# Optimization experiments

Measured on AMD Instinct MI355X. Metric: run time of the kernel, lower is better.

## Reference

```python
import jax, jax.numpy as jnp
import numpy as np
from jax import lax

B, N, C, RED = 8, 2048, 1024, 4
GN_EPS = 1e-5


def setup_inputs() -> dict:
    key = jax.random.key(0)
    ks = jax.random.split(key, 8)
    s = lambda k, shp, sc: jax.random.normal(k, shp, jnp.float32) * sc
    return dict(
        x=jax.random.normal(ks[0], (B, N, C), jnp.float32),
        qkv_w=s(ks[1], (C, 3 * C), 0.02),
        c1=jnp.float32(0.01 ** 2),
        c2=jnp.float32(0.03 ** 2),
        conv1_w=s(ks[2], (4, 1, 3), 0.3),      # OIH
        gn_g=jnp.ones(4, jnp.float32),
        gn_b=jnp.zeros(4, jnp.float32),
        conv2_w=s(ks[3], (1, 4, 3), 0.3),      # OIH
        conv2_b=jnp.zeros(1, jnp.float32),
        ch_w1=s(ks[4], (C, C // RED), 0.02),
        ch_b1=jnp.zeros(C // RED, jnp.float32),
        ch_w2=s(ks[5], (C // RED, C), 0.02),
        ch_b2=jnp.zeros(C, jnp.float32),
        proj_w=s(ks[6], (C, C), 0.02),
        proj_b=jnp.zeros(C, jnp.float32),
    )


def _conv1d(x, w):  # x:[B,Cin,N], w:[O,I,3], pad=1
    return lax.conv_general_dilated(x, w, (1,), [(1, 1)],
                                    dimension_numbers=('NCH', 'OIH', 'NCH'))


def _ode_func(A, conv1_w, gn_g, gn_b, conv2_w, conv2_b):
    # A: [B,N] -> Conv1d(1,4) -> GroupNorm(2,4) -> ReLU -> Conv1d(4,1)
    h = _conv1d(A[:, None, :], conv1_w)                 # [B,4,N]
    b, _, n = h.shape
    hg = h.reshape(b, 2, 2, n)                          # 2 groups of 2 channels
    mu = hg.mean((2, 3), keepdims=True)
    var = hg.var((2, 3), keepdims=True)
    h = ((hg - mu) * lax.rsqrt(var + GN_EPS)).reshape(b, 4, n)
    h = jax.nn.relu(h * gn_g[None, :, None] + gn_b[None, :, None])
    y = _conv1d(h, conv2_w) + conv2_b[None, :, None]    # [B,1,N]
    return y[:, 0, :]


def reference(x, qkv_w, c1, c2, conv1_w, gn_g, gn_b, conv2_w, conv2_b,
              ch_w1, ch_b1, ch_w2, ch_b2, proj_w, proj_b):
    Bx, Nx, Cx = x.shape
    qkv = (x @ qkv_w).reshape(Bx, Nx, 3, Cx)
    q, k, v = qkv[..., 0, :], qkv[..., 1, :], qkv[..., 2, :]

    # SSIM-style per-token statistics over the channel dim
    mu_q = q.mean(-1, keepdims=True)
    mu_k = k.mean(-1, keepdims=True)
    dq, dk = q - mu_q, k - mu_k
    inv_cm1 = 1.0 / (Cx - 1)
    sigma_qk = (dq * dk).sum(-1, keepdims=True) * inv_cm1
    sigma_q2 = (dq * dq).sum(-1, keepdims=True) * inv_cm1
    sigma_k2 = (dk * dk).sum(-1, keepdims=True) * inv_cm1
    num = (2 * mu_q * mu_k + c1) * (2 * sigma_qk + c2)
    den = (mu_q ** 2 + mu_k ** 2 + c1) * (sigma_q2 + sigma_k2 + c2)
    attn_base = ((num / (den + 1e-7)) ** 2)[..., 0]     # [B,N]

    # explicit-Euler integration over t = linspace(0,1,2) -> one step, dt=1
    steps = 2
    ts = jnp.linspace(0.0, 1.0, steps)
    dts = ts[1:] - ts[:-1]

    def step(A, dt):
        return A + dt * _ode_func(A, conv1_w, gn_g, gn_b, conv2_w, conv2_b), None

    A, _ = lax.scan(step, attn_base, dts)
    final_a = jax.nn.sigmoid(A)                         # [B,N]
    weights = jax.nn.softmax(final_a, axis=1)           # softmax over tokens

    # channel gating from mean token
    m = x.mean(axis=1, keepdims=True)                   # [B,1,C]
    ch_w = jax.nn.sigmoid(jax.nn.relu(m @ ch_w1 + ch_b1) @ ch_w2 + ch_b2)

    out_low = weights[..., None] * v * ch_w             # [B,N,C]
    return out_low @ proj_w + proj_b
```

## Files before the change

kernel.cpp:

```cpp
#include <hip/hip_runtime.h>

typedef __attribute__((ext_vector_type(8))) short short8;
typedef __attribute__((ext_vector_type(4))) short short4v;
typedef __attribute__((ext_vector_type(4))) float floatx4;

__device__ __forceinline__ unsigned short f2bf(float f) {
    unsigned u = __float_as_uint(f);
    u = u + 0x7fffu + ((u >> 16) & 1u);
    return (unsigned short)(u >> 16);
}

__device__ __forceinline__ void gl_lds16(const void* g, void* l) {
    __builtin_amdgcn_global_load_lds((const __attribute__((address_space(1))) void*)g,
                                     (__attribute__((address_space(3))) void*)l, 16, 0, 0);
}

__global__ __launch_bounds__(256) void convmean_kernel(const float* __restrict__ x,
                                                       short* __restrict__ xb,
                                                       float* __restrict__ part) {
    int bid = blockIdx.x;
    int b = bid >> 6, nch = bid & 63;
    int tid = threadIdx.x;
    size_t base = ((size_t)b * 2048 + nch * 32) * 1024;
    float s0 = 0.f, s1 = 0.f, s2 = 0.f, s3 = 0.f;
    int c0 = tid * 4;
    for (int r = 0; r < 32; r++) {
        const float* rp = x + base + (size_t)r * 1024 + c0;
        float4 v = *(const float4*)rp;
        s0 += v.x; s1 += v.y; s2 += v.z; s3 += v.w;
        short4v o;
        o[0] = (short)f2bf(v.x); o[1] = (short)f2bf(v.y);
        o[2] = (short)f2bf(v.z); o[3] = (short)f2bf(v.w);
        *(short4v*)(xb + base + (size_t)r * 1024 + c0) = o;
    }
    float* pp = part + ((size_t)b * 64 + nch) * 1024 + c0;
    float4 ps; ps.x = s0; ps.y = s1; ps.z = s2; ps.w = s3;
    *(float4*)pp = ps;
}

__global__ __launch_bounds__(256) void transpose_conv_kernel(const float* __restrict__ w_qkv,
                                                             short* __restrict__ qkvT,
                                                             const float* __restrict__ w_proj,
                                                             short* __restrict__ projT) {
    __shared__ float t[64][65];
    int bx = blockIdx.x;
    const float* in; short* out; int C; bool is_qkv;
    int c0, r0 = blockIdx.y * 64;
    if (bx < 48) { in = w_qkv; out = qkvT; C = 3072; c0 = bx * 64; is_qkv = true; }
    else         { in = w_proj; out = projT; C = 1024; c0 = (bx - 48) * 64; is_qkv = false; }
    int tid = threadIdx.x;
#pragma unroll
    for (int l = 0; l < 16; l++) {
        int idx = l * 256 + tid;
        int rr = idx >> 6, cc = idx & 63;
        t[rr][cc] = in[(size_t)(r0 + rr) * C + c0 + cc];
    }
    __syncthreads();
#pragma unroll
    for (int l = 0; l < 16; l++) {
        int idx = l * 256 + tid;
        int rr = idx >> 6, cc = idx & 63;
        int ro = c0 + rr;
        int rnew = ro;
        if (is_qkv) {
            if (ro < 1024) rnew = 2 * ro;
            else if (ro < 2048) rnew = 2 * (ro - 1024) + 1;
        }
        out[(size_t)rnew * 1024 + r0 + cc] = (short)f2bf(t[cc][rr]);
    }
}

__global__ __launch_bounds__(256) void ch_kernel(const float* __restrict__ part,
                                                 const float* __restrict__ w1,
                                                 const float* __restrict__ b1,
                                                 const float* __restrict__ w2,
                                                 const float* __restrict__ b2,
                                                 float* __restrict__ ch) {
    int b = blockIdx.x >> 3, cg = blockIdx.x & 7;
    int tid = threadIdx.x;
    __shared__ float mrow[1024];
    __shared__ float hid[256];
    for (int i = tid; i < 1024; i += 256) {
        float s = 0.f;
        for (int j = 0; j < 64; j++) s += part[((size_t)b * 64 + j) * 1024 + i];
        mrow[i] = s * (1.f / 2048.f);
    }
    __syncthreads();
    {
        float s0 = 0.f, s1 = 0.f, s2 = 0.f, s3 = 0.f;
        for (int i = 0; i < 1024; i += 4) {
            s0 += mrow[i] * w1[(size_t)i * 256 + tid];
            s1 += mrow[i + 1] * w1[(size_t)(i + 1) * 256 + tid];
            s2 += mrow[i + 2] * w1[(size_t)(i + 2) * 256 + tid];
            s3 += mrow[i + 3] * w1[(size_t)(i + 3) * 256 + tid];
        }
        hid[tid] = fmaxf((s0 + s1) + (s2 + s3) + b1[tid], 0.f);
    }
    __syncthreads();
    if (tid < 128) {
        int c = cg * 128 + tid;
        float s0 = 0.f, s1 = 0.f, s2 = 0.f, s3 = 0.f;
        for (int j = 0; j < 256; j += 4) {
            s0 += hid[j] * w2[(size_t)j * 1024 + c];
            s1 += hid[j + 1] * w2[(size_t)(j + 1) * 1024 + c];
            s2 += hid[j + 2] * w2[(size_t)(j + 2) * 1024 + c];
            s3 += hid[j + 3] * w2[(size_t)(j + 3) * 1024 + c];
        }
        float s = (s0 + s1) + (s2 + s3) + b2[c];
        ch[(size_t)b * 1024 + c] = 1.f / (1.f + expf(-s));
    }
}


#define LDB4()                                                                          \
    {                                                                                   \
        _Pragma("unroll")                                                               \
        for (int jj = 0; jj < 4; jj++)                                                  \
            bfr[jj] = *(const short8*)(Bs_ + (wn * 64 + jj * 16 + ar) * 32 + swq);      \
    }

#define PH(qq, STAGE)                                                                   \
    {                                                                                   \
        short8 a0 = *(const short8*)(As_ + (wm * 128 + ((qq)*2 + 0) * 16 + ar) * 32 + swq); \
        short8 a1 = *(const short8*)(As_ + (wm * 128 + ((qq)*2 + 1) * 16 + ar) * 32 + swq); \
        STAGE;                                                                          \
        asm volatile("s_barrier" ::: "memory");                                         \
        __builtin_amdgcn_sched_barrier(0);                                              \
        __builtin_amdgcn_s_setprio(1);                                                  \
        _Pragma("unroll")                                                               \
        for (int jj = 0; jj < 4; jj++)                                                  \
            acc[(qq)*2 + 0][jj] =                                                       \
                __builtin_amdgcn_mfma_f32_16x16x32_bf16(a0, bfr[jj], acc[(qq)*2 + 0][jj], 0, 0, 0); \
        _Pragma("unroll")                                                               \
        for (int jj = 0; jj < 4; jj++)                                                  \
            acc[(qq)*2 + 1][jj] =                                                       \
                __builtin_amdgcn_mfma_f32_16x16x32_bf16(a1, bfr[jj], acc[(qq)*2 + 1][jj], 0, 0, 0); \
        __builtin_amdgcn_s_setprio(0);                                                  \
    }

#define TILE_BODY(T, SA0, SA1, SB0, SB1)                                                \
    {                                                                                   \
        const short* As_ = ASf + ((T) & 3) * 8192;                                      \
        const short* Bs_ = BSf + ((T) & 3) * 8192;                                      \
        LDB4();                                                                         \
        PH(0, SA0);                                                                     \
        asm volatile("s_barrier" ::: "memory");                                         \
        PH(1, SA1);                                                                     \
        asm volatile("s_barrier" ::: "memory");                                         \
        PH(2, SB0);                                                                     \
        asm volatile("s_barrier" ::: "memory");                                         \
        PH(3, SB1);                                                                     \
    }

__global__ __launch_bounds__(512, 2) void gemm_qkv_kernel(const short* __restrict__ A,
                                                          const short* __restrict__ BT,
                                                          short* __restrict__ vbuf,
                                                          const float* __restrict__ ch,
                                                          float* __restrict__ part2)
{
    __shared__ __align__(16) short ASf[4 * 8192];
    __shared__ __align__(16) short BSf[4 * 8192];
    const int tid = threadIdx.x;
    const int wave = tid >> 6, lane = tid & 63;
    const int id = blockIdx.x;
    const int xcd = id & 7, j = id >> 3;
    const int bn = j % 12;
    const int bmg = j / 12;
    const int bm = bmg * 8 + xcd;
    const int wm = wave >> 2, wn = wave & 3;
    const int ar = lane & 15, quad = lane >> 4;
    const int swq = (quad ^ ((ar >> 1) & 3)) * 8;

    const int swzk = ((lane & 3) ^ ((lane >> 3) & 3)) * 8;
    const short* Ag = A + (size_t)(bm * 256 + wave * 32 + (lane >> 2)) * 1024 + swzk;
    const short* Bg = BT + (size_t)(bn * 256 + wave * 32 + (lane >> 2)) * 1024 + swzk;
    short* ASw = ASf + wave * 1024;
    short* BSw = BSf + wave * 1024;

    floatx4 acc[8][4];
    floatx4 zero = {0.f, 0.f, 0.f, 0.f};
#pragma unroll
    for (int i = 0; i < 8; i++)
#pragma unroll
        for (int jj = 0; jj < 4; jj++) acc[i][jj] = zero;

    auto stA0 = [&](int t) { gl_lds16(Ag + t * 32, ASw + (t & 3) * 8192); };
    auto stA1 = [&](int t) { gl_lds16(Ag + (size_t)16 * 1024 + t * 32, ASw + (t & 3) * 8192 + 512); };
    auto stB0 = [&](int t) { gl_lds16(Bg + t * 32, BSw + (t & 3) * 8192); };
    auto stB1 = [&](int t) { gl_lds16(Bg + (size_t)16 * 1024 + t * 32, BSw + (t & 3) * 8192 + 512); };

    short8 bfr[4];

    stA0(0); stA1(0); stB0(0); stB1(0);
    stA0(1); stA1(1); stB0(1); stB1(1);
    asm volatile("s_waitcnt vmcnt(4)" ::: "memory");
    asm volatile("s_barrier" ::: "memory");
    for (int t = 0; t < 30; ++t) {
        TILE_BODY(t, stA0(t + 2), stA1(t + 2), stB0(t + 2), stB1(t + 2));
        asm volatile("s_waitcnt vmcnt(4)" ::: "memory");
        asm volatile("s_barrier" ::: "memory");
    }
    TILE_BODY(30, , , , );
    asm volatile("s_waitcnt vmcnt(0)" ::: "memory");
    asm volatile("s_barrier" ::: "memory");
    TILE_BODY(31, , , , );
    __syncthreads();

    if (bn < 8) {
        float* sb = (float*)ASf;
#pragma unroll
        for (int i = 0; i < 8; i++) {
            float st[4][5];
#pragma unroll
            for (int r = 0; r < 4; r++)
#pragma unroll
                for (int f = 0; f < 5; f++) st[r][f] = 0.f;
#pragma unroll
            for (int jj = 0; jj < 4; jj++) {
#pragma unroll
                for (int r = 0; r < 4; r++) {
                    float val = acc[i][jj][r];
                    float other = __shfl_xor(val, 1);
                    float q = (lane & 1) ? other : val;
                    float kv = (lane & 1) ? val : other;
                    st[r][0] += q; st[r][1] += kv;
                    st[r][2] += q * q; st[r][3] += kv * kv; st[r][4] += q * kv;
                }
            }
#pragma unroll
            for (int r = 0; r < 4; r++)
#pragma unroll
                for (int f = 0; f < 5; f++) {
                    float v = st[r][f];
                    v += __shfl_xor(v, 2);
                    v += __shfl_xor(v, 4);
                    v += __shfl_xor(v, 8);
                    st[r][f] = v;
                }
            if ((lane & 15) == 0) {
#pragma unroll
                for (int r = 0; r < 4; r++)
#pragma unroll
                    for (int f = 0; f < 5; f++)
                        sb[(size_t)(wn * 256 + wm * 128 + i * 16 + quad * 4 + r) * 5 + f] = st[r][f];
            }
        }
        __syncthreads();
        if (tid < 256) {
#pragma unroll
            for (int f = 0; f < 5; f++) {
                float s = sb[(size_t)(0 * 256 + tid) * 5 + f] + sb[(size_t)(1 * 256 + tid) * 5 + f] +
                          sb[(size_t)(2 * 256 + tid) * 5 + f] + sb[(size_t)(3 * 256 + tid) * 5 + f];
                part2[(size_t)(bn * 5 + f) * 16384 + bm * 256 + tid] = s;
            }
        }
    } else {
        const int batch = bm >> 3;
        const int vcol0 = bn * 256 - 2048 + wn * 64;
        short* pbuf = (short*)ASf + wave * 1024;
        float cw[4];
#pragma unroll
        for (int jj = 0; jj < 4; jj++) cw[jj] = ch[(size_t)batch * 1024 + vcol0 + jj * 16 + ar];
#pragma unroll
        for (int i = 0; i < 8; i++) {
#pragma unroll
            for (int jj = 0; jj < 4; jj++)
#pragma unroll
                for (int r = 0; r < 4; r++)
                    pbuf[(quad * 4 + r) * 64 + jj * 16 + ar] = (short)f2bf(acc[i][jj][r] * cw[jj]);
#pragma unroll
            for (int p = 0; p < 2; p++) {
                int idx = p * 512 + lane * 8;
                short8 vv = *(const short8*)(pbuf + idx);
                int grow = bm * 256 + wm * 128 + i * 16 + (idx >> 6);
                int gcol = vcol0 + (idx & 63);
                *(short8*)(vbuf + (size_t)grow * 1024 + gcol) = vv;
            }
        }
    }
}

__global__ __launch_bounds__(256) void finalize_kernel(const float* __restrict__ part2,
                                                       const float* __restrict__ c1p,
                                                       const float* __restrict__ c2p,
                                                       float* __restrict__ attn) {
    int row = blockIdx.x * 256 + threadIdx.x;
    float s[5] = {0.f, 0.f, 0.f, 0.f, 0.f};
#pragma unroll
    for (int slot = 0; slot < 8; slot++)
#pragma unroll
        for (int f = 0; f < 5; f++)
            s[f] += part2[(size_t)((slot * 5 + f) << 14) + row];
    const float C = 1024.f, invcm1 = 1.f / 1023.f;
    float c1 = *c1p, c2 = *c2p;
    float muq = s[0] / C, muk = s[1] / C;
    float sigqk = (s[4] - C * muq * muk) * invcm1;
    float sigq2 = (s[2] - C * muq * muq) * invcm1;
    float sigk2 = (s[3] - C * muk * muk) * invcm1;
    float num = (2.f * muq * muk + c1) * (2.f * sigqk + c2);
    float den = (muq * muq + muk * muk + c1) * (sigq2 + sigk2 + c2);
    float r = num / (den + 1e-7f);
    attn[row] = r * r;
}

__device__ __forceinline__ float blk_sum(float v, float* buf) {
#pragma unroll
    for (int m = 1; m < 64; m <<= 1) v += __shfl_xor(v, m);
    int wave = threadIdx.x >> 6;
    if ((threadIdx.x & 63) == 0) buf[wave] = v;
    __syncthreads();
    float r = buf[0] + buf[1] + buf[2] + buf[3];
    __syncthreads();
    return r;
}
__device__ __forceinline__ float blk_max(float v, float* buf) {
#pragma unroll
    for (int m = 1; m < 64; m <<= 1) v = fmaxf(v, __shfl_xor(v, m));
    int wave = threadIdx.x >> 6;
    if ((threadIdx.x & 63) == 0) buf[wave] = v;
    __syncthreads();
    float r = fmaxf(fmaxf(buf[0], buf[1]), fmaxf(buf[2], buf[3]));
    __syncthreads();
    return r;
}

__global__ __launch_bounds__(256) void ode_softmax_kernel(const float* __restrict__ attn,
                                                          const float* __restrict__ w1,
                                                          const float* __restrict__ gng,
                                                          const float* __restrict__ gnb,
                                                          const float* __restrict__ w2,
                                                          const float* __restrict__ b2,
                                                          float* __restrict__ wgt) {
    int b = blockIdx.x, tid = threadIdx.x;
    __shared__ float A0[2048];
    __shared__ float H[4][2048];
    __shared__ float rbuf[4];
    for (int i = tid; i < 2048; i += 256) A0[i] = attn[(size_t)b * 2048 + i];
    __syncthreads();
    float w1l[12], w2l[12];
#pragma unroll
    for (int i = 0; i < 12; i++) { w1l[i] = w1[i]; w2l[i] = w2[i]; }
    float gg[4], gb[4];
#pragma unroll
    for (int c = 0; c < 4; c++) { gg[c] = gng[c]; gb[c] = gnb[c]; }

    float s0 = 0.f, ss0 = 0.f, s1 = 0.f, ss1 = 0.f;
    for (int i = tid; i < 2048; i += 256) {
        float le = (i > 0) ? A0[i - 1] : 0.f;
        float mi = A0[i];
        float ri = (i < 2047) ? A0[i + 1] : 0.f;
#pragma unroll
        for (int c = 0; c < 4; c++) {
            float h = w1l[c * 3] * le + w1l[c * 3 + 1] * mi + w1l[c * 3 + 2] * ri;
            H[c][i] = h;
            if (c < 2) { s0 += h; ss0 += h * h; } else { s1 += h; ss1 += h * h; }
        }
    }
    s0 = blk_sum(s0, rbuf);
    ss0 = blk_sum(ss0, rbuf);
    s1 = blk_sum(s1, rbuf);
    ss1 = blk_sum(ss1, rbuf);
    float mu0 = s0 / 4096.f, var0 = ss0 / 4096.f - mu0 * mu0;
    float mu1 = s1 / 4096.f, var1 = ss1 / 4096.f - mu1 * mu1;
    float is0 = 1.f / sqrtf(var0 + 1e-5f);
    float is1 = 1.f / sqrtf(var1 + 1e-5f);

    for (int i = tid; i < 2048; i += 256) {
#pragma unroll
        for (int c = 0; c < 4; c++) {
            float inv = (c < 2) ? is0 : is1;
            float mu = (c < 2) ? mu0 : mu1;
            float v = (H[c][i] - mu) * inv * gg[c] + gb[c];
            H[c][i] = fmaxf(v, 0.f);
        }
    }
    __syncthreads();

    float bias2 = b2[0];
    float myfa[8];
    float lmax = -1e30f;
#pragma unroll
    for (int ii = 0; ii < 8; ii++) {
        int i = tid + ii * 256;
        float y = bias2;
#pragma unroll
        for (int c = 0; c < 4; c++) {
            float le = (i > 0) ? H[c][i - 1] : 0.f;
            float mi = H[c][i];
            float ri = (i < 2047) ? H[c][i + 1] : 0.f;
            y += w2l[c * 3] * le + w2l[c * 3 + 1] * mi + w2l[c * 3 + 2] * ri;
        }
        float Av = A0[i] + y;
        float fa = 1.f / (1.f + expf(-Av));
        myfa[ii] = fa;
        lmax = fmaxf(lmax, fa);
    }
    float gmax = blk_max(lmax, rbuf);
    float lsum = 0.f;
#pragma unroll
    for (int ii = 0; ii < 8; ii++) {
        myfa[ii] = expf(myfa[ii] - gmax);
        lsum += myfa[ii];
    }
    float gsum = blk_sum(lsum, rbuf);
    float inv = 1.f / gsum;
#pragma unroll
    for (int ii = 0; ii < 8; ii++) wgt[(size_t)b * 2048 + tid + ii * 256] = myfa[ii] * inv;
}

__global__ __launch_bounds__(512, 2) void gemm_out_kernel(const short* __restrict__ vbuf,
                                                          const short* __restrict__ BT,
                                                          const float* __restrict__ wgt,
                                                          const float* __restrict__ pb,
                                                          float* __restrict__ Out)
{
    __shared__ __align__(16) short ASf[4 * 8192];
    __shared__ __align__(16) short BSf[4 * 8192];
    const int tid = threadIdx.x;
    const int wave = tid >> 6, lane = tid & 63;
    const int id = blockIdx.x;
    const int xcd = id & 7, j = id >> 3;
    const int bn = j & 3;
    const int bmg = j >> 2;
    const int bm = bmg * 8 + xcd;
    const int wm = wave >> 2, wn = wave & 3;
    const int ar = lane & 15, quad = lane >> 4;
    const int swq = (quad ^ ((ar >> 1) & 3)) * 8;

    const int swzk = ((lane & 3) ^ ((lane >> 3) & 3)) * 8;
    const short* Ag = vbuf + (size_t)(bm * 256 + wave * 32 + (lane >> 2)) * 1024 + swzk;
    const short* Bg = BT + (size_t)(bn * 256 + wave * 32 + (lane >> 2)) * 1024 + swzk;
    short* ASw = ASf + wave * 1024;
    short* BSw = BSf + wave * 1024;

    floatx4 acc[8][4];
    floatx4 zero = {0.f, 0.f, 0.f, 0.f};
#pragma unroll
    for (int i = 0; i < 8; i++)
#pragma unroll
        for (int jj = 0; jj < 4; jj++) acc[i][jj] = zero;

    auto stA0 = [&](int t) { gl_lds16(Ag + t * 32, ASw + (t & 3) * 8192); };
    auto stA1 = [&](int t) { gl_lds16(Ag + (size_t)16 * 1024 + t * 32, ASw + (t & 3) * 8192 + 512); };
    auto stB0 = [&](int t) { gl_lds16(Bg + t * 32, BSw + (t & 3) * 8192); };
    auto stB1 = [&](int t) { gl_lds16(Bg + (size_t)16 * 1024 + t * 32, BSw + (t & 3) * 8192 + 512); };

    short8 bfr[4];

    stA0(0); stA1(0); stB0(0); stB1(0);
    stA0(1); stA1(1); stB0(1); stB1(1);
    asm volatile("s_waitcnt vmcnt(4)" ::: "memory");
    asm volatile("s_barrier" ::: "memory");
    for (int t = 0; t < 30; ++t) {
        TILE_BODY(t, stA0(t + 2), stA1(t + 2), stB0(t + 2), stB1(t + 2));
        asm volatile("s_waitcnt vmcnt(4)" ::: "memory");
        asm volatile("s_barrier" ::: "memory");
    }
    TILE_BODY(30, , , , );
    asm volatile("s_waitcnt vmcnt(0)" ::: "memory");
    asm volatile("s_barrier" ::: "memory");
    TILE_BODY(31, , , , );
    __syncthreads();

    const int row0 = bm * 256 + wm * 128;
    const int col0 = bn * 256 + wn * 64;
    float* obuf = (float*)ASf + wave * 1024;
#pragma unroll
    for (int i = 0; i < 8; i++) {
#pragma unroll
        for (int jj = 0; jj < 4; jj++) {
            float bias = pb[col0 + jj * 16 + ar];
#pragma unroll
            for (int r = 0; r < 4; r++) {
                int grow = row0 + i * 16 + quad * 4 + r;
                obuf[(quad * 4 + r) * 64 + jj * 16 + ar] = wgt[grow] * acc[i][jj][r] + bias;
            }
        }
#pragma unroll
        for (int p = 0; p < 4; p++) {
            int idx = p * 256 + lane * 4;
            float4 vv = *(const float4*)(obuf + idx);
            int grow = row0 + i * 16 + (idx >> 6);
            int gcol = col0 + (idx & 63);
            *(float4*)(Out + (size_t)grow * 1024 + gcol) = vv;
        }
    }
}

extern "C" void kernel_launch(void* const* d_in, const int* in_sizes, int n_in,
                              void* d_out, int out_size, void* d_ws, size_t ws_size,
                              hipStream_t stream) {
    const float* x       = (const float*)d_in[0];
    const float* qkv_w   = (const float*)d_in[1];
    const float* c1      = (const float*)d_in[2];
    const float* c2      = (const float*)d_in[3];
    const float* conv1_w = (const float*)d_in[4];
    const float* gn_g    = (const float*)d_in[5];
    const float* gn_b    = (const float*)d_in[6];
    const float* conv2_w = (const float*)d_in[7];
    const float* conv2_b = (const float*)d_in[8];
    const float* ch_w1   = (const float*)d_in[9];
    const float* ch_b1   = (const float*)d_in[10];
    const float* ch_w2   = (const float*)d_in[11];
    const float* ch_b2   = (const float*)d_in[12];
    const float* proj_w  = (const float*)d_in[13];
    const float* proj_b  = (const float*)d_in[14];
    float* out = (float*)d_out;

    size_t off = 0;
    char* base = (char*)d_ws;
    auto carve = [&](size_t bytes) -> char* {
        char* p = base + off;
        off += (bytes + 255) & ~(size_t)255;
        return p;
    };
    short* x_bf  = (short*)carve((size_t)16384 * 1024 * 2);
    short* qkvT  = (short*)carve((size_t)3072 * 1024 * 2);
    short* projT = (short*)carve((size_t)1024 * 1024 * 2);
    short* vbuf  = (short*)carve((size_t)16384 * 1024 * 2);
    float* part2 = (float*)carve((size_t)80 * 16384 * 4);
    float* attn  = (float*)carve((size_t)16384 * 4);
    float* wgt   = (float*)carve((size_t)16384 * 4);
    float* part  = (float*)carve((size_t)8 * 64 * 1024 * 4);
    float* chw   = (float*)carve((size_t)8 * 1024 * 4);

    convmean_kernel<<<512, 256, 0, stream>>>(x, x_bf, part);
    transpose_conv_kernel<<<dim3(64, 16), 256, 0, stream>>>(qkv_w, qkvT, proj_w, projT);
    ch_kernel<<<64, 256, 0, stream>>>(part, ch_w1, ch_b1, ch_w2, ch_b2, chw);
    gemm_qkv_kernel<<<768, 512, 0, stream>>>(x_bf, qkvT, vbuf, chw, part2);
    finalize_kernel<<<64, 256, 0, stream>>>(part2, c1, c2, attn);
    ode_softmax_kernel<<<8, 256, 0, stream>>>(attn, conv1_w, gn_g, gn_b, conv2_w, conv2_b, wgt);
    gemm_out_kernel<<<256, 512, 0, stream>>>(vbuf, projT, wgt, proj_b, out);
}
```

Before: 406.3 us.

## Shrink GEMM tiles to 128x256 with double buffering for higher occupancy

Both GEMM kernels move from a 256x256 block tile with a 4-stage LDS ring and phased MFMA/load interleaving to a 128x256 tile with a simple 2-stage double buffer. Each iteration issues the next stage, waits, then runs all 16 MFMAs per wave. Launch bounds ask for 4 blocks per CU and the grid doubles. The aim is better occupancy and more blocks to spread across CUs, paid for with lower arithmetic intensity per tile, more total global traffic for B, and less software pipelining depth.

```diff
diff --git a/kernel.cpp b/kernel.cpp
--- a/kernel.cpp
+++ b/kernel.cpp
@@ -112,54 +112,33 @@
 }
 
 
-#define LDB4()                                                                          \
+#define KLOOP_BODY(T)                                                                   \
     {                                                                                   \
+        const short* As_ = SH + ((T) & 1) * 4096;                                       \
+        const short* Bs_ = SH + 8192 + ((T) & 1) * 8192;                                \
         _Pragma("unroll")                                                               \
         for (int jj = 0; jj < 4; jj++)                                                  \
             bfr[jj] = *(const short8*)(Bs_ + (wn * 64 + jj * 16 + ar) * 32 + swq);      \
-    }
-
-#define PH(qq, STAGE)                                                                   \
-    {                                                                                   \
-        short8 a0 = *(const short8*)(As_ + (wm * 128 + ((qq)*2 + 0) * 16 + ar) * 32 + swq); \
-        short8 a1 = *(const short8*)(As_ + (wm * 128 + ((qq)*2 + 1) * 16 + ar) * 32 + swq); \
-        STAGE;                                                                          \
-        asm volatile("s_barrier" ::: "memory");                                         \
-        __builtin_amdgcn_sched_barrier(0);                                              \
+        _Pragma("unroll")                                                               \
+        for (int ii = 0; ii < 4; ii++)                                                  \
+            af[ii] = *(const short8*)(As_ + (wm * 64 + ii * 16 + ar) * 32 + swq);       \
         __builtin_amdgcn_s_setprio(1);                                                  \
         _Pragma("unroll")                                                               \
-        for (int jj = 0; jj < 4; jj++)                                                  \
-            acc[(qq)*2 + 0][jj] =                                                       \
-                __builtin_amdgcn_mfma_f32_16x16x32_bf16(a0, bfr[jj], acc[(qq)*2 + 0][jj], 0, 0, 0); \
-        _Pragma("unroll")                                                               \
-        for (int jj = 0; jj < 4; jj++)                                                  \
-            acc[(qq)*2 + 1][jj] =                                                       \
-                __builtin_amdgcn_mfma_f32_16x16x32_bf16(a1, bfr[jj], acc[(qq)*2 + 1][jj], 0, 0, 0); \
+        for (int ii = 0; ii < 4; ii++)                                                  \
+            _Pragma("unroll")                                                           \
+            for (int jj = 0; jj < 4; jj++)                                              \
+                acc[ii][jj] =                                                           \
+                    __builtin_amdgcn_mfma_f32_16x16x32_bf16(af[ii], bfr[jj], acc[ii][jj], 0, 0, 0); \
         __builtin_amdgcn_s_setprio(0);                                                  \
     }
 
-#define TILE_BODY(T, SA0, SA1, SB0, SB1)                                                \
-    {                                                                                   \
-        const short* As_ = ASf + ((T) & 3) * 8192;                                      \
-        const short* Bs_ = BSf + ((T) & 3) * 8192;                                      \
-        LDB4();                                                                         \
-        PH(0, SA0);                                                                     \
-        asm volatile("s_barrier" ::: "memory");                                         \
-        PH(1, SA1);                                                                     \
-        asm volatile("s_barrier" ::: "memory");                                         \
-        PH(2, SB0);                                                                     \
-        asm volatile("s_barrier" ::: "memory");                                         \
-        PH(3, SB1);                                                                     \
-    }
-
-__global__ __launch_bounds__(512, 2) void gemm_qkv_kernel(const short* __restrict__ A,
+__global__ __launch_bounds__(512, 4) void gemm_qkv_kernel(const short* __restrict__ A,
                                                           const short* __restrict__ BT,
                                                           short* __restrict__ vbuf,
                                                           const float* __restrict__ ch,
                                                           float* __restrict__ part2)
 {
-    __shared__ __align__(16) short ASf[4 * 8192];
-    __shared__ __align__(16) short BSf[4 * 8192];
+    __shared__ __align__(16) short SH[2 * 4096 + 2 * 8192];
     const int tid = threadIdx.x;
     const int wave = tid >> 6, lane = tid & 63;
     const int id = blockIdx.x;
@@ -172,44 +151,44 @@
     const int swq = (quad ^ ((ar >> 1) & 3)) * 8;
 
     const int swzk = ((lane & 3) ^ ((lane >> 3) & 3)) * 8;
-    const short* Ag = A + (size_t)(bm * 256 + wave * 32 + (lane >> 2)) * 1024 + swzk;
+    const short* Ag = A + (size_t)(bm * 128 + wave * 16 + (lane >> 2)) * 1024 + swzk;
     const short* Bg = BT + (size_t)(bn * 256 + wave * 32 + (lane >> 2)) * 1024 + swzk;
-    short* ASw = ASf + wave * 1024;
-    short* BSw = BSf + wave * 1024;
-
-    floatx4 acc[8][4];
+    short* ASw = SH + wave * 512;
+    short* BSw = SH + 8192 + wave * 1024;
+
+    floatx4 acc[4][4];
     floatx4 zero = {0.f, 0.f, 0.f, 0.f};
 #pragma unroll
-    for (int i = 0; i < 8; i++)
+    for (int i = 0; i < 4; i++)
 #pragma unroll
         for (int jj = 0; jj < 4; jj++) acc[i][jj] = zero;
 
-    auto stA0 = [&](int t) { gl_lds16(Ag + t * 32, ASw + (t & 3) * 8192); };
-    auto stA1 = [&](int t) { gl_lds16(Ag + (size_t)16 * 1024 + t * 32, ASw + (t & 3) * 8192 + 512); };
-    auto stB0 = [&](int t) { gl_lds16(Bg + t * 32, BSw + (t & 3) * 8192); };
-    auto stB1 = [&](int t) { gl_lds16(Bg + (size_t)16 * 1024 + t * 32, BSw + (t & 3) * 8192 + 512); };
-
-    short8 bfr[4];
-
-    stA0(0); stA1(0); stB0(0); stB1(0);
-    stA0(1); stA1(1); stB0(1); stB1(1);
-    asm volatile("s_waitcnt vmcnt(4)" ::: "memory");
-    asm volatile("s_barrier" ::: "memory");
-    for (int t = 0; t < 30; ++t) {
-        TILE_BODY(t, stA0(t + 2), stA1(t + 2), stB0(t + 2), stB1(t + 2));
-        asm volatile("s_waitcnt vmcnt(4)" ::: "memory");
+    auto stage = [&](int t) {
+        const int sa = (t & 1) * 4096, sb2 = (t & 1) * 8192, ko = t * 32;
+        gl_lds16(Ag + ko, ASw + sa);
+        gl_lds16(Bg + ko, BSw + sb2);
+        gl_lds16(Bg + (size_t)16 * 1024 + ko, BSw + sb2 + 512);
+    };
+
+    short8 af[4], bfr[4];
+
+    stage(0);
+    for (int t = 0; t < 31; ++t) {
+        stage(t + 1);
+        asm volatile("s_waitcnt vmcnt(3)" ::: "memory");
         asm volatile("s_barrier" ::: "memory");
-    }
-    TILE_BODY(30, , , , );
+        KLOOP_BODY(t);
+        asm volatile("s_barrier" ::: "memory");
+    }
     asm volatile("s_waitcnt vmcnt(0)" ::: "memory");
     asm volatile("s_barrier" ::: "memory");
-    TILE_BODY(31, , , , );
+    KLOOP_BODY(31);
     __syncthreads();
 
     if (bn < 8) {
-        float* sb = (float*)ASf;
-#pragma unroll
-        for (int i = 0; i < 8; i++) {
+        float* sb = (float*)SH;
+#pragma unroll
+        for (int i = 0; i < 4; i++) {
             float st[4][5];
 #pragma unroll
             for (int r = 0; r < 4; r++)
@@ -242,27 +221,27 @@
                 for (int r = 0; r < 4; r++)
 #pragma unroll
                     for (int f = 0; f < 5; f++)
-                        sb[(size_t)(wn * 256 + wm * 128 + i * 16 + quad * 4 + r) * 5 + f] = st[r][f];
+                        sb[(size_t)(wn * 128 + wm * 64 + i * 16 + quad * 4 + r) * 5 + f] = st[r][f];
             }
         }
         __syncthreads();
-        if (tid < 256) {
+        if (tid < 128) {
 #pragma unroll
             for (int f = 0; f < 5; f++) {
-                float s = sb[(size_t)(0 * 256 + tid) * 5 + f] + sb[(size_t)(1 * 256 + tid) * 5 + f] +
-                          sb[(size_t)(2 * 256 + tid) * 5 + f] + sb[(size_t)(3 * 256 + tid) * 5 + f];
-                part2[(size_t)(bn * 5 + f) * 16384 + bm * 256 + tid] = s;
+                float s = sb[(size_t)(0 * 128 + tid) * 5 + f] + sb[(size_t)(1 * 128 + tid) * 5 + f] +
+                          sb[(size_t)(2 * 128 + tid) * 5 + f] + sb[(size_t)(3 * 128 + tid) * 5 + f];
+                part2[(size_t)(bn * 5 + f) * 16384 + bm * 128 + tid] = s;
             }
         }
     } else {
-        const int batch = bm >> 3;
+        const int batch = bm >> 4;
         const int vcol0 = bn * 256 - 2048 + wn * 64;
-        short* pbuf = (short*)ASf + wave * 1024;
+        short* pbuf = SH + wave * 1024;
         float cw[4];
 #pragma unroll
         for (int jj = 0; jj < 4; jj++) cw[jj] = ch[(size_t)batch * 1024 + vcol0 + jj * 16 + ar];
 #pragma unroll
-        for (int i = 0; i < 8; i++) {
+        for (int i = 0; i < 4; i++) {
 #pragma unroll
             for (int jj = 0; jj < 4; jj++)
 #pragma unroll
@@ -272,7 +251,7 @@
             for (int p = 0; p < 2; p++) {
                 int idx = p * 512 + lane * 8;
                 short8 vv = *(const short8*)(pbuf + idx);
-                int grow = bm * 256 + wm * 128 + i * 16 + (idx >> 6);
+                int grow = bm * 128 + wm * 64 + i * 16 + (idx >> 6);
                 int gcol = vcol0 + (idx & 63);
                 *(short8*)(vbuf + (size_t)grow * 1024 + gcol) = vv;
             }
@@ -408,14 +387,13 @@
     for (int ii = 0; ii < 8; ii++) wgt[(size_t)b * 2048 + tid + ii * 256] = myfa[ii] * inv;
 }
 
-__global__ __launch_bounds__(512, 2) void gemm_out_kernel(const short* __restrict__ vbuf,
+__global__ __launch_bounds__(512, 4) void gemm_out_kernel(const short* __restrict__ vbuf,
                                                           const short* __restrict__ BT,
                                                           const float* __restrict__ wgt,
                                                           const float* __restrict__ pb,
                                                           float* __restrict__ Out)
 {
-    __shared__ __align__(16) short ASf[4 * 8192];
-    __shared__ __align__(16) short BSf[4 * 8192];
+    __shared__ __align__(16) short SH[2 * 4096 + 2 * 8192];
     const int tid = threadIdx.x;
     const int wave = tid >> 6, lane = tid & 63;
     const int id = blockIdx.x;
@@ -428,45 +406,45 @@
     const int swq = (quad ^ ((ar >> 1) & 3)) * 8;
 
     const int swzk = ((lane & 3) ^ ((lane >> 3) & 3)) * 8;
-    const short* Ag = vbuf + (size_t)(bm * 256 + wave * 32 + (lane >> 2)) * 1024 + swzk;
+    const short* Ag = vbuf + (size_t)(bm * 128 + wave * 16 + (lane >> 2)) * 1024 + swzk;
     const short* Bg = BT + (size_t)(bn * 256 + wave * 32 + (lane >> 2)) * 1024 + swzk;
-    short* ASw = ASf + wave * 1024;
-    short* BSw = BSf + wave * 1024;
-
-    floatx4 acc[8][4];
+    short* ASw = SH + wave * 512;
+    short* BSw = SH + 8192 + wave * 1024;
+
+    floatx4 acc[4][4];
     floatx4 zero = {0.f, 0.f, 0.f, 0.f};
 #pragma unroll
-    for (int i = 0; i < 8; i++)
+    for (int i = 0; i < 4; i++)
 #pragma unroll
         for (int jj = 0; jj < 4; jj++) acc[i][jj] = zero;
 
-    auto stA0 = [&](int t) { gl_lds16(Ag + t * 32, ASw + (t & 3) * 8192); };
-    auto stA1 = [&](int t) { gl_lds16(Ag + (size_t)16 * 1024 + t * 32, ASw + (t & 3) * 8192 + 512); };
-    auto stB0 = [&](int t) { gl_lds16(Bg + t * 32, BSw + (t & 3) * 8192); };
-    auto stB1 = [&](int t) { gl_lds16(Bg + (size_t)16 * 1024 + t * 32, BSw + (t & 3) * 8192 + 512); };
-
-    short8 bfr[4];
-
-    stA0(0); stA1(0); stB0(0); stB1(0);
-    stA0(1); stA1(1); stB0(1); stB1(1);
-    asm volatile("s_waitcnt vmcnt(4)" ::: "memory");
-    asm volatile("s_barrier" ::: "memory");
-    for (int t = 0; t < 30; ++t) {
-        TILE_BODY(t, stA0(t + 2), stA1(t + 2), stB0(t + 2), stB1(t + 2));
-        asm volatile("s_waitcnt vmcnt(4)" ::: "memory");
+    auto stage = [&](int t) {
+        const int sa = (t & 1) * 4096, sb2 = (t & 1) * 8192, ko = t * 32;
+        gl_lds16(Ag + ko, ASw + sa);
+        gl_lds16(Bg + ko, BSw + sb2);
+        gl_lds16(Bg + (size_t)16 * 1024 + ko, BSw + sb2 + 512);
+    };
+
+    short8 af[4], bfr[4];
+
+    stage(0);
+    for (int t = 0; t < 31; ++t) {
+        stage(t + 1);
+        asm volatile("s_waitcnt vmcnt(3)" ::: "memory");
         asm volatile("s_barrier" ::: "memory");
-    }
-    TILE_BODY(30, , , , );
+        KLOOP_BODY(t);
+        asm volatile("s_barrier" ::: "memory");
+    }
     asm volatile("s_waitcnt vmcnt(0)" ::: "memory");
     asm volatile("s_barrier" ::: "memory");
-    TILE_BODY(31, , , , );
-    __syncthreads();
-
-    const int row0 = bm * 256 + wm * 128;
+    KLOOP_BODY(31);
+    __syncthreads();
+
+    const int row0 = bm * 128 + wm * 64;
     const int col0 = bn * 256 + wn * 64;
-    float* obuf = (float*)ASf + wave * 1024;
-#pragma unroll
-    for (int i = 0; i < 8; i++) {
+    float* obuf = (float*)SH + wave * 1024;
+#pragma unroll
+    for (int i = 0; i < 4; i++) {
 #pragma unroll
         for (int jj = 0; jj < 4; jj++) {
             float bias = pb[col0 + jj * 16 + ar];
@@ -527,8 +505,8 @@
     convmean_kernel<<<512, 256, 0, stream>>>(x, x_bf, part);
     transpose_conv_kernel<<<dim3(64, 16), 256, 0, stream>>>(qkv_w, qkvT, proj_w, projT);
     ch_kernel<<<64, 256, 0, stream>>>(part, ch_w1, ch_b1, ch_w2, ch_b2, chw);
-    gemm_qkv_kernel<<<768, 512, 0, stream>>>(x_bf, qkvT, vbuf, chw, part2);
+    gemm_qkv_kernel<<<1536, 512, 0, stream>>>(x_bf, qkvT, vbuf, chw, part2);
     finalize_kernel<<<64, 256, 0, stream>>>(part2, c1, c2, attn);
     ode_softmax_kernel<<<8, 256, 0, stream>>>(attn, conv1_w, gn_g, gn_b, conv2_w, conv2_b, wgt);
-    gemm_out_kernel<<<256, 512, 0, stream>>>(vbuf, projT, wgt, proj_b, out);
-}
+    gemm_out_kernel<<<512, 512, 0, stream>>>(vbuf, projT, wgt, proj_b, out);
+}
```

Measured after the change: 405.5 us. About the same (-0.2%).
